# Performance work log

Measured on AMD Instinct MI355X. Metric: run time of the kernel, lower is better.

## Reference

```python
import jax, jax.numpy as jnp
import numpy as np


def soft_threshold24(w):
    """2:4 soft-threshold along the last dim: in each contiguous group of 4,
    zero the two smallest magnitudes and shrink the two largest by the
    second-smallest magnitude (sign(w) * relu(|w| - t))."""
    M, N = w.shape
    g = w.reshape(M, N // 4, 4)
    a = jnp.abs(g)
    thr = jnp.sort(a, axis=-1)[..., 1:2]  # 2nd-smallest magnitude per group
    s = jnp.sign(g) * jnp.maximum(a - thr, 0.0)
    return s.reshape(M, N)


def mm_fp16(a, b):
    """fake_fp8_mm: cast operands to fp16, accumulate in fp32."""
    return jnp.matmul(a.astype(jnp.float16), b.astype(jnp.float16),
                      preferred_element_type=jnp.float32)


def setup_inputs() -> dict:
    key = jax.random.key(0)
    k0, k1, k2, k3 = jax.random.split(key, 4)
    B, S, D, R = 4, 2048, 2048, 512
    return {
        "x": jax.random.normal(k0, (B, S, D), jnp.float32),
        "weight_in": jax.random.normal(k1, (D, R), jnp.float32) * 0.02,
        "weight_out": jax.random.normal(k2, (D, R), jnp.float32) * 0.02,
        "bias": jax.random.normal(k3, (D,), jnp.float32) * 0.01,
        "sparse_scale_in": jnp.array(1.0, jnp.float32),
        "sparse_scale_out": jnp.array(1.0, jnp.float32),
    }


def reference(x, weight_in, weight_out, bias, sparse_scale_in, sparse_scale_out):
    B, S, D = x.shape
    # stage 1: x @ sparse24(weight_in) * scale_in  -> [B,S,R]
    win_s = soft_threshold24(weight_in) * sparse_scale_in          # [D, R]
    h = mm_fp16(x.reshape(-1, D), win_s)                            # [B*S, R] fp32
    # stage 2: h @ sparse24(weight_out.T) * scale_out + bias -> [B,S,D]
    wout_s = soft_threshold24(weight_out.T) * sparse_scale_out      # [R, D]
    out = mm_fp16(h, wout_s) + bias                                 # [B*S, D]
    return out.reshape(B, S, D)
```

## Files before the change

### kernel.cpp

```cpp
#include <hip/hip_runtime.h>

typedef _Float16 f16;
typedef _Float16 f16x8 __attribute__((ext_vector_type(8)));
typedef float f32x4 __attribute__((ext_vector_type(4)));

#define BK 32

__device__ __forceinline__ void g2l16(const f16* g, f16* l) {
    __builtin_amdgcn_global_load_lds(
        (const __attribute__((address_space(1))) void*)g,
        (__attribute__((address_space(3))) void*)l, 16, 0, 0);
}

__device__ __forceinline__ float soft1(float a, float thr, float w, float s) {
    return copysignf(fmaxf(a - thr, 0.0f), w) * s;
}

__device__ __forceinline__ float thr4(float a0, float a1, float a2, float a3) {
    float lo01 = fminf(a0, a1), hi01 = fmaxf(a0, a1);
    float lo23 = fminf(a2, a3), hi23 = fmaxf(a2, a3);
    return fminf(fmaxf(lo01, lo23), fminf(hi01, hi23));
}

__global__ __launch_bounds__(256) void prep_kernel(
    const float* __restrict__ x, f16* __restrict__ xh, int n8,
    const float* __restrict__ Wi, f16* __restrict__ winT, const float* __restrict__ sci,
    const float* __restrict__ Wo, f16* __restrict__ woutT, const float* __restrict__ sco,
    int D, int R, int nCastB, int nSpInB)
{
    int b = blockIdx.x;
    int tid = threadIdx.x;
    if (b < nCastB) {
        int i = b * 256 + tid;
        if (i < n8) {
            float4 a = reinterpret_cast<const float4*>(x)[2 * i];
            float4 c = reinterpret_cast<const float4*>(x)[2 * i + 1];
            f16x8 o = {(f16)a.x, (f16)a.y, (f16)a.z, (f16)a.w,
                       (f16)c.x, (f16)c.y, (f16)c.z, (f16)c.w};
            reinterpret_cast<f16x8*>(xh)[i] = o;
        }
    } else if (b < nCastB + nSpInB) {
        int t = (b - nCastB) * 256 + tid;
        int RG = R >> 2;
        if (t >= RG * D) return;
        int rg = t / D, d = t - rg * D;
        float s = *sci;
        float4 w = *reinterpret_cast<const float4*>(Wi + (size_t)d * R + rg * 4);
        float a0 = fabsf(w.x), a1 = fabsf(w.y), a2 = fabsf(w.z), a3 = fabsf(w.w);
        float thr = thr4(a0, a1, a2, a3);
        size_t base = (size_t)(rg * 4) * D + d;
        winT[base]                 = (f16)soft1(a0, thr, w.x, s);
        winT[base + D]             = (f16)soft1(a1, thr, w.y, s);
        winT[base + 2 * (size_t)D] = (f16)soft1(a2, thr, w.z, s);
        winT[base + 3 * (size_t)D] = (f16)soft1(a3, thr, w.w, s);
    } else {
        int t = (b - nCastB - nSpInB) * 256 + tid;
        if (t >= (D >> 2) * R) return;
        int dg = t / R, r = t - dg * R;
        float s = *sco;
        size_t i0 = (size_t)(dg * 4) * R + r;
        float w0 = Wo[i0], w1 = Wo[i0 + R], w2 = Wo[i0 + 2 * (size_t)R], w3 = Wo[i0 + 3 * (size_t)R];
        float a0 = fabsf(w0), a1 = fabsf(w1), a2 = fabsf(w2), a3 = fabsf(w3);
        float thr = thr4(a0, a1, a2, a3);
        woutT[i0]                 = (f16)soft1(a0, thr, w0, s);
        woutT[i0 + R]             = (f16)soft1(a1, thr, w1, s);
        woutT[i0 + 2 * (size_t)R] = (f16)soft1(a2, thr, w2, s);
        woutT[i0 + 3 * (size_t)R] = (f16)soft1(a3, thr, w3, s);
    }
}

template <int TBM, int TBN, typename OT, bool BIAS>
__global__ __launch_bounds__(256) void gemm_bt(
    const f16* __restrict__ A, const f16* __restrict__ Bt, OT* __restrict__ C,
    const float* __restrict__ bias, int M, int N, int K)
{
    constexpr int MI = TBM / 32;
    constexpr int NF = TBN / 32;
    constexpr int HM = TBM / 2;
    constexpr int HN = TBN / 2;
    __shared__ f16 As[TBM * BK];
    __shared__ f16 Bs[TBN * BK];

    const int tid  = threadIdx.x;
    const int lane = tid & 63;
    const int w    = tid >> 6;
    const int wm   = w & 1;
    const int wn   = w >> 1;
    const int l16  = lane & 15;
    const int quad = lane >> 4;
    const int bm = blockIdx.y * TBM;
    const int bn = blockIdx.x * TBN;

    const int srow = lane >> 2;
    const int scol = (lane & 3) * 8;
    const f16* gA = A  + (size_t)(bm + w * (TBM / 4) + srow) * K + scol;
    const f16* gB = Bt + (size_t)(bn + w * (TBN / 4) + srow) * K + scol;
    f16* lA = &As[(w * (TBM / 4)) * BK];
    f16* lB = &Bs[(w * (TBN / 4)) * BK];

    f32x4 acc[MI][NF] = {};

    for (int k0 = 0; k0 < K; k0 += BK) {
#pragma unroll
        for (int i = 0; i < TBM / 64; ++i)
            g2l16(gA + k0 + i * 16 * (size_t)K, lA + i * 16 * BK);
#pragma unroll
        for (int i = 0; i < TBN / 64; ++i)
            g2l16(gB + k0 + i * 16 * (size_t)K, lB + i * 16 * BK);
        __syncthreads();

        f16x8 af[MI], bf[NF];
#pragma unroll
        for (int m = 0; m < MI; ++m)
            af[m] = *reinterpret_cast<const f16x8*>(&As[(wm * HM + m * 16 + l16) * BK + quad * 8]);
#pragma unroll
        for (int n = 0; n < NF; ++n)
            bf[n] = *reinterpret_cast<const f16x8*>(&Bs[(wn * HN + n * 16 + l16) * BK + quad * 8]);
#pragma unroll
        for (int m = 0; m < MI; ++m)
#pragma unroll
            for (int n = 0; n < NF; ++n)
                acc[m][n] = __builtin_amdgcn_mfma_f32_16x16x32_f16(af[m], bf[n], acc[m][n], 0, 0, 0);
        __syncthreads();
    }

#pragma unroll
    for (int m = 0; m < MI; ++m) {
        int row_base = bm + wm * HM + m * 16 + quad * 4;
#pragma unroll
        for (int n = 0; n < NF; ++n) {
            int col = bn + wn * HN + n * 16 + l16;
            float b = BIAS ? bias[col] : 0.0f;
#pragma unroll
            for (int r = 0; r < 4; ++r) {
                float v = acc[m][n][r];
                size_t idx = (size_t)(row_base + r) * N + col;
                if constexpr (BIAS) C[idx] = (OT)(v + b);
                else                C[idx] = (OT)v;
            }
        }
    }
}

extern "C" void kernel_launch(void* const* d_in, const int* in_sizes, int n_in,
                              void* d_out, int out_size, void* d_ws, size_t ws_size,
                              hipStream_t stream)
{
    const float* x      = (const float*)d_in[0];
    const float* w_in   = (const float*)d_in[1];
    const float* w_out  = (const float*)d_in[2];
    const float* bias   = (const float*)d_in[3];
    const float* sc_in  = (const float*)d_in[4];
    const float* sc_out = (const float*)d_in[5];

    const int D = in_sizes[3];
    const int R = in_sizes[1] / D;
    const int M = in_sizes[0] / D;

    f16* winT  = (f16*)d_ws;
    f16* woutT = winT + (size_t)R * D;
    f16* h     = woutT + (size_t)D * R;
    f16* xh    = h + (size_t)M * R;
    float* out = (float*)d_out;

    const int n8 = M * D / 8;
    const int nCastB  = (n8 + 255) / 256;
    const int nSpInB  = ((R / 4) * D + 255) / 256;
    const int nSpOutB = ((D / 4) * R + 255) / 256;
    prep_kernel<<<nCastB + nSpInB + nSpOutB, 256, 0, stream>>>(
        x, xh, n8, w_in, winT, sc_in, w_out, woutT, sc_out, D, R, nCastB, nSpInB);

    gemm_bt<64, 64, f16, false><<<dim3(R / 64, M / 64), 256, 0, stream>>>(
        xh, winT, h, nullptr, M, R, D);
    gemm_bt<64, 128, float, true><<<dim3(D / 128, M / 64), 256, 0, stream>>>(
        h, woutT, out, bias, M, D, R);
}
```

Before: 194.8 us.

## Double-buffer LDS tiles, remap blocks across XCDs, and widen the first GEMM tile

The GEMM kernel now keeps two LDS stages. It issues the async global-to-LDS loads for the next K slice before running the MFMAs on the current one, so the loop needs one barrier per step instead of two. The 2D grid becomes a 1D grid whose block index is permuted in groups of eight, so neighbouring tiles land on the same XCD and share L2. The first GEMM switches from 64x64 to 64x128 tiles. Costs are twice the shared memory, a loop that assumes an even number of K steps, and fewer blocks for the first GEMM.

```diff
diff --git a/kernel.cpp b/kernel.cpp
--- a/kernel.cpp
+++ b/kernel.cpp
@@ -78,8 +78,8 @@
     constexpr int NF = TBN / 32;
     constexpr int HM = TBM / 2;
     constexpr int HN = TBN / 2;
-    __shared__ f16 As[TBM * BK];
-    __shared__ f16 Bs[TBN * BK];
+    __shared__ f16 As[2][TBM * BK];
+    __shared__ f16 Bs[2][TBN * BK];
 
     const int tid  = threadIdx.x;
     const int lane = tid & 63;
@@ -88,41 +88,67 @@
     const int wn   = w >> 1;
     const int l16  = lane & 15;
     const int quad = lane >> 4;
-    const int bm = blockIdx.y * TBM;
-    const int bn = blockIdx.x * TBN;
+
+    const int nbx = N / TBN;
+    const int nb  = gridDim.x;
+    int d = blockIdx.x;
+    int wgid = ((nb & 7) == 0) ? ((d & 7) * (nb >> 3) + (d >> 3)) : d;
+    int by = wgid / nbx;
+    int bx = wgid - by * nbx;
+    const int bm = by * TBM;
+    const int bn = bx * TBN;
 
     const int srow = lane >> 2;
     const int scol = (lane & 3) * 8;
     const f16* gA = A  + (size_t)(bm + w * (TBM / 4) + srow) * K + scol;
     const f16* gB = Bt + (size_t)(bn + w * (TBN / 4) + srow) * K + scol;
-    f16* lA = &As[(w * (TBM / 4)) * BK];
-    f16* lB = &Bs[(w * (TBN / 4)) * BK];
 
     f32x4 acc[MI][NF] = {};
 
-    for (int k0 = 0; k0 < K; k0 += BK) {
+    auto STAGE = [&](int buf, int k0) {
+        f16* lA = &As[buf][(w * (TBM / 4)) * BK];
+        f16* lB = &Bs[buf][(w * (TBN / 4)) * BK];
 #pragma unroll
         for (int i = 0; i < TBM / 64; ++i)
             g2l16(gA + k0 + i * 16 * (size_t)K, lA + i * 16 * BK);
 #pragma unroll
         for (int i = 0; i < TBN / 64; ++i)
             g2l16(gB + k0 + i * 16 * (size_t)K, lB + i * 16 * BK);
-        __syncthreads();
-
+        __builtin_amdgcn_sched_barrier(0);
+    };
+
+    auto COMPUTE = [&](int buf) {
         f16x8 af[MI], bf[NF];
 #pragma unroll
         for (int m = 0; m < MI; ++m)
-            af[m] = *reinterpret_cast<const f16x8*>(&As[(wm * HM + m * 16 + l16) * BK + quad * 8]);
+            af[m] = *reinterpret_cast<const f16x8*>(
+                &As[buf][(wm * HM + m * 16 + l16) * BK + quad * 8]);
 #pragma unroll
         for (int n = 0; n < NF; ++n)
-            bf[n] = *reinterpret_cast<const f16x8*>(&Bs[(wn * HN + n * 16 + l16) * BK + quad * 8]);
+            bf[n] = *reinterpret_cast<const f16x8*>(
+                &Bs[buf][(wn * HN + n * 16 + l16) * BK + quad * 8]);
 #pragma unroll
         for (int m = 0; m < MI; ++m)
 #pragma unroll
             for (int n = 0; n < NF; ++n)
                 acc[m][n] = __builtin_amdgcn_mfma_f32_16x16x32_f16(af[m], bf[n], acc[m][n], 0, 0, 0);
+    };
+
+    const int nk = K / BK;
+    STAGE(0, 0);
+    __syncthreads();
+    for (int t = 0; t < nk - 2; t += 2) {
+        STAGE(1, (t + 1) * BK);
+        COMPUTE(0);
+        __syncthreads();
+        STAGE(0, (t + 2) * BK);
+        COMPUTE(1);
         __syncthreads();
     }
+    STAGE(1, (nk - 1) * BK);
+    COMPUTE(0);
+    __syncthreads();
+    COMPUTE(1);
 
 #pragma unroll
     for (int m = 0; m < MI; ++m) {
@@ -170,8 +196,8 @@
     prep_kernel<<<nCastB + nSpInB + nSpOutB, 256, 0, stream>>>(
         x, xh, n8, w_in, winT, sc_in, w_out, woutT, sc_out, D, R, nCastB, nSpInB);
 
-    gemm_bt<64, 64, f16, false><<<dim3(R / 64, M / 64), 256, 0, stream>>>(
+    gemm_bt<64, 128, f16, false><<<(R / 128) * (M / 64), 256, 0, stream>>>(
         xh, winT, h, nullptr, M, R, D);
-    gemm_bt<64, 128, float, true><<<dim3(D / 128, M / 64), 256, 0, stream>>>(
+    gemm_bt<64, 128, float, true><<<(D / 128) * (M / 64), 256, 0, stream>>>(
         h, woutT, out, bias, M, D, R);
 }
```

Measured after the change: 183.3 us. -5.9%, faster.
